# Kernel optimization log

Measured on AMD Instinct MI355X. Metric: run time of the kernel, lower is better.

The kernel has to match this reference:

```python
import jax, jax.numpy as jnp
import numpy as np

N = 50000
E = 800000
D_IN = 64
D_E = 32
H = 128
EPS = 1e-5


def _seg_mean(msgs, dst, n):
    s = jax.ops.segment_sum(msgs, dst, num_segments=n)
    c = jax.ops.segment_sum(jnp.ones((dst.shape[0], 1), msgs.dtype), dst, num_segments=n)
    return s / jnp.maximum(c, 1.0)


def _bn(h, g, b, m, v):
    return g * (h - m) * jax.lax.rsqrt(v + EPS) + b


def setup_inputs() -> dict:
    key = jax.random.key(0)
    ks = jax.random.split(key, 32)
    inp = {
        "x": jax.random.normal(ks[0], (N, D_IN), jnp.float32),
        "edge_index_0": jax.random.randint(ks[1], (2, E), 0, N),
        "edge_index_1": jax.random.randint(ks[2], (2, E), 0, N),
        "edge_index_2": jax.random.randint(ks[3], (2, E), 0, N),
        "edge_attr_0": jax.random.normal(ks[4], (E, D_E), jnp.float32),
        # conv1: Linear(D_IN + D_E -> H)
        "W1": jax.random.normal(ks[5], (H, D_IN + D_E), jnp.float32) * 0.1,
        "b1": jnp.zeros((H,), jnp.float32),
        "g1": jnp.ones((H,), jnp.float32), "be1": jnp.zeros((H,), jnp.float32),
        "m1": jax.random.normal(ks[6], (H,), jnp.float32) * 0.1,
        "v1": jax.random.uniform(ks[7], (H,), jnp.float32) + 0.5,
        # SAGEConv2: lin_l (bias) on aggregated neighbors + lin_r (no bias) on self
        "Wl2": jax.random.normal(ks[8], (H, H), jnp.float32) * 0.1,
        "bl2": jnp.zeros((H,), jnp.float32),
        "Wr2": jax.random.normal(ks[9], (H, H), jnp.float32) * 0.1,
        "g2": jnp.ones((H,), jnp.float32), "be2": jnp.zeros((H,), jnp.float32),
        "m2": jax.random.normal(ks[10], (H,), jnp.float32) * 0.1,
        "v2": jax.random.uniform(ks[11], (H,), jnp.float32) + 0.5,
        # SAGEConv3
        "Wl3": jax.random.normal(ks[12], (H, H), jnp.float32) * 0.1,
        "bl3": jnp.zeros((H,), jnp.float32),
        "Wr3": jax.random.normal(ks[13], (H, H), jnp.float32) * 0.1,
        "g3": jnp.ones((H,), jnp.float32), "be3": jnp.zeros((H,), jnp.float32),
        "m3": jax.random.normal(ks[14], (H,), jnp.float32) * 0.1,
        "v3": jax.random.uniform(ks[15], (H,), jnp.float32) + 0.5,
        # mlp: Linear(H + D_IN -> 64) -> ReLU -> Linear(64 -> 1)
        "W4": jax.random.normal(ks[16], (64, H + D_IN), jnp.float32) * 0.1,
        "b4": jnp.zeros((64,), jnp.float32),
        "W5": jax.random.normal(ks[17], (1, 64), jnp.float32) * 0.1,
        "b5": jnp.zeros((1,), jnp.float32),
    }
    return inp


def reference(x, edge_index_0, edge_index_1, edge_index_2, edge_attr_0,
              W1, b1, g1, be1, m1, v1,
              Wl2, bl2, Wr2, g2, be2, m2, v2,
              Wl3, bl3, Wr3, g3, be3, m3, v3,
              W4, b4, W5, b5):
    n = x.shape[0]
    init = x
    # conv1: gather x_j + edge_attr, concat, linear, mean scatter, relu (update)
    msg = jnp.concatenate([x[edge_index_0[0]], edge_attr_0], axis=-1) @ W1.T + b1  # [E,H]
    h = jax.nn.relu(_seg_mean(msg, edge_index_0[1], n))
    h = jax.nn.relu(_bn(h, g1, be1, m1, v1))  # dropout: eval (identity)
    # conv2: SAGEConv = lin_l(mean_j x_j) + lin_r(x)
    agg = _seg_mean(h[edge_index_1[0]], edge_index_1[1], n)
    h = agg @ Wl2.T + bl2 + h @ Wr2.T
    h = jax.nn.relu(_bn(h, g2, be2, m2, v2))
    # conv3
    agg = _seg_mean(h[edge_index_2[0]], edge_index_2[1], n)
    h = agg @ Wl3.T + bl3 + h @ Wr3.T
    h = jax.nn.relu(_bn(h, g3, be3, m3, v3))
    # readout mlp on [h, initial_embedding]
    z = jnp.concatenate([h, init], axis=1)
    z = jax.nn.relu(z @ W4.T + b4)
    out = (z @ W5.T + b5).squeeze(-1)  # [N]
    return out
```

## Files before the change

### kernel.cpp

```cpp
#include <hip/hip_runtime.h>
#include <hip/hip_bf16.h>
#include <stdint.h>

#define NN 50000
#define NE 800000
#define EPS 1e-5f

#define KB 196
#define SH 8
#define NPB 256
#define RCAP 4500
#define PT2 2048
#define NT2 391
#define GP3 (3 * NT2)
#define GCVT ((3290112 + 255) / 256)

typedef __attribute__((ext_vector_type(8))) short bf16x8;
typedef __attribute__((ext_vector_type(4))) float floatx4;

static __device__ __forceinline__ float bf2f(unsigned int u){
  union { unsigned int i; float f; } c; c.i = u << 16; return c.f;
}
static __device__ __forceinline__ unsigned short f2bf(float f){
  union { float f; unsigned int i; } c; c.f = f;
  unsigned int x = c.i;
  return (unsigned short)((x + 0x7fffu + ((x >> 16) & 1u)) >> 16);
}

#define CVT_X   3200000
#define CVT_W1  3212288
#define CVT_WL2 3228672
#define CVT_WR2 3245056
#define CVT_WL3 3261440
#define CVT_WR3 3277824
#define CVT_END 3290112

__global__ void k_part3cvt(const int* __restrict__ ei0, const int* __restrict__ ei1,
                           const int* __restrict__ ei2, int* __restrict__ gcur,
                           int2* __restrict__ rec,
                           const float* __restrict__ x,  const float* __restrict__ W1,
                           const float* __restrict__ Wl2, const float* __restrict__ Wr2,
                           const float* __restrict__ Wl3, const float* __restrict__ Wr3,
                           const float* __restrict__ W4,
                           unsigned short* __restrict__ xb,  unsigned short* __restrict__ W1b,
                           unsigned short* __restrict__ Wl2b, unsigned short* __restrict__ Wr2b,
                           unsigned short* __restrict__ Wl3b, unsigned short* __restrict__ Wr3b,
                           unsigned short* __restrict__ W4b){
  __shared__ int2 stage[PT2];
  __shared__ int hist[KB], ex[KB], cur[KB], gbase[KB];
  __shared__ int part[256];
  __shared__ int tot;
  int tid = threadIdx.x;

  if(blockIdx.x >= GP3){
    int i = (blockIdx.x - GP3) * 256 + tid;
    if(i >= CVT_END) return;
    if(i < CVT_X)        xb[i] = f2bf(x[i]);
    else if(i < CVT_W1)  W1b[i - CVT_X]    = f2bf(W1[i - CVT_X]);
    else if(i < CVT_WL2) Wl2b[i - CVT_W1]  = f2bf(Wl2[i - CVT_W1]);
    else if(i < CVT_WR2) Wr2b[i - CVT_WL2] = f2bf(Wr2[i - CVT_WL2]);
    else if(i < CVT_WL3) Wl3b[i - CVT_WR2] = f2bf(Wl3[i - CVT_WR2]);
    else if(i < CVT_WR3) Wr3b[i - CVT_WL3] = f2bf(Wr3[i - CVT_WL3]);
    else                 W4b[i - CVT_WR3]  = f2bf(W4[i - CVT_WR3]);
    return;
  }

  int layer = blockIdx.x % 3;
  int tile = (blockIdx.x / 3) * PT2;
  const int* ei = (layer == 0) ? ei0 : ((layer == 1) ? ei1 : ei2);
  int2* recL = rec + (size_t)layer * KB * RCAP;
  int* gcurL = gcur + layer * KB;
  for(int i = tid; i < KB; i += 256) hist[i] = 0;
  __syncthreads();
  int dst[8], pay[8];
  #pragma unroll
  for(int j = 0; j < 8; j++){
    int e = tile + j * 256 + tid;
    if(e < NE){
      dst[j] = ei[NE + e];
      pay[j] = (layer == 0) ? e : ei[e];
      atomicAdd(&hist[dst[j] >> SH], 1);
    }
    else dst[j] = -1;
  }
  __syncthreads();
  int c0 = (tid < KB) ? hist[tid] : 0;
  part[tid] = c0;
  __syncthreads();
  for(int d = 1; d < 256; d <<= 1){
    int v = (tid >= d) ? part[tid - d] : 0;
    __syncthreads();
    part[tid] += v;
    __syncthreads();
  }
  if(tid < KB){
    int e = part[tid] - c0;
    ex[tid] = e; cur[tid] = e;
    gbase[tid] = atomicAdd(&gcurL[tid], c0);
  }
  if(tid == 255) tot = part[255];
  __syncthreads();
  #pragma unroll
  for(int j = 0; j < 8; j++){
    if(dst[j] >= 0){
      int b = dst[j] >> SH;
      int s = atomicAdd(&cur[b], 1);
      stage[s] = make_int2(dst[j], pay[j]);
    }
  }
  __syncthreads();
  for(int s = tid; s < tot; s += 256){
    int2 r = stage[s];
    int b = r.x >> SH;
    recL[b * RCAP + gbase[b] + (s - ex[b])] = r;
  }
}

__global__ void k_build3(const int2* __restrict__ rec, const int* __restrict__ gcnt,
                         const int* __restrict__ ei0,
                         int2* __restrict__ adj2, int* __restrict__ adjI1, int* __restrict__ adjI2,
                         int* __restrict__ rowbeg3, int* __restrict__ deg3){
  __shared__ int cnt[NPB], cur2[NPB];
  __shared__ int part[256];
  int layer = blockIdx.x % 3;
  int b = blockIdx.x / 3;
  int tid = threadIdx.x;
  int n0 = b << SH;
  int nr = gcnt[layer * KB + b];
  const int2* r = rec + ((size_t)layer * KB + b) * RCAP;
  cnt[tid] = 0;
  __syncthreads();
  for(int k = tid; k < nr; k += 256) atomicAdd(&cnt[r[k].x - n0], 1);
  __syncthreads();
  int c0 = cnt[tid];
  part[tid] = c0;
  __syncthreads();
  for(int d = 1; d < 256; d <<= 1){
    int v = (tid >= d) ? part[tid - d] : 0;
    __syncthreads();
    part[tid] += v;
    __syncthreads();
  }
  int base = part[tid] - c0;
  cur2[tid] = base;
  __syncthreads();
  int n = n0 + tid;
  if(n < NN){ rowbeg3[layer * NN + n] = b * RCAP + base; deg3[layer * NN + n] = c0; }
  for(int k = tid; k < nr; k += 256){
    int2 q = r[k];
    int p = atomicAdd(&cur2[q.x - n0], 1);
    if(layer == 0)      adj2[b * RCAP + p]  = make_int2(ei0[q.y], q.y);
    else if(layer == 1) adjI1[b * RCAP + p] = q.y;
    else                adjI2[b * RCAP + p] = q.y;
  }
}

__global__ void k_aggXE(const int* __restrict__ rowbeg, const int* __restrict__ deg,
                        const int2* __restrict__ adj2,
                        const unsigned short* __restrict__ xb, const float* __restrict__ ea,
                        unsigned short* __restrict__ agg){
  int w = (blockIdx.x * blockDim.x + threadIdx.x) >> 6;
  int lane = threadIdx.x & 63;
  if(w >= NN) return;
  int sub = lane >> 4, li = lane & 15;
  int r0 = rowbeg[w], dg = deg[w], r1 = r0 + dg;
  float acc[8] = {0.f,0.f,0.f,0.f,0.f,0.f,0.f,0.f};
  for(int k = r0; k < r1; k += 8){
    int e0 = k + sub, e1 = k + 4 + sub;
    int i0 = e0 < r1 ? e0 : r1 - 1;
    int i1 = e1 < r1 ? e1 : r1 - 1;
    float m0 = e0 < r1 ? 1.f : 0.f;
    float m1 = e1 < r1 ? 1.f : 0.f;
    int2 a0 = adj2[i0], a1 = adj2[i1];
    if(li < 8){
      uint4 v0 = *(const uint4*)(xb + (size_t)a0.x * 64 + li * 8);
      uint4 v1 = *(const uint4*)(xb + (size_t)a1.x * 64 + li * 8);
      acc[0] += m0 * bf2f(v0.x & 0xffffu); acc[1] += m0 * bf2f(v0.x >> 16);
      acc[2] += m0 * bf2f(v0.y & 0xffffu); acc[3] += m0 * bf2f(v0.y >> 16);
      acc[4] += m0 * bf2f(v0.z & 0xffffu); acc[5] += m0 * bf2f(v0.z >> 16);
      acc[6] += m0 * bf2f(v0.w & 0xffffu); acc[7] += m0 * bf2f(v0.w >> 16);
      acc[0] += m1 * bf2f(v1.x & 0xffffu); acc[1] += m1 * bf2f(v1.x >> 16);
      acc[2] += m1 * bf2f(v1.y & 0xffffu); acc[3] += m1 * bf2f(v1.y >> 16);
      acc[4] += m1 * bf2f(v1.z & 0xffffu); acc[5] += m1 * bf2f(v1.z >> 16);
      acc[6] += m1 * bf2f(v1.w & 0xffffu); acc[7] += m1 * bf2f(v1.w >> 16);
    } else {
      int j = li - 8;
      float4 p0 = *(const float4*)(ea + (size_t)a0.y * 32 + j * 4);
      float4 p1 = *(const float4*)(ea + (size_t)a1.y * 32 + j * 4);
      acc[0] += m0 * p0.x; acc[1] += m0 * p0.y;
      acc[2] += m0 * p0.z; acc[3] += m0 * p0.w;
      acc[0] += m1 * p1.x; acc[1] += m1 * p1.y;
      acc[2] += m1 * p1.z; acc[3] += m1 * p1.w;
    }
  }
  #pragma unroll
  for(int d = 16; d < 64; d <<= 1){
    #pragma unroll
    for(int i = 0; i < 8; i++) acc[i] += __shfl_xor(acc[i], d, 64);
  }
  if(sub == 0){
    float inv = 1.0f / (float)(dg > 0 ? dg : 1);
    if(li < 8){
      unsigned int q0 = (unsigned int)f2bf(acc[0]*inv) | ((unsigned int)f2bf(acc[1]*inv) << 16);
      unsigned int q1 = (unsigned int)f2bf(acc[2]*inv) | ((unsigned int)f2bf(acc[3]*inv) << 16);
      unsigned int q2 = (unsigned int)f2bf(acc[4]*inv) | ((unsigned int)f2bf(acc[5]*inv) << 16);
      unsigned int q3 = (unsigned int)f2bf(acc[6]*inv) | ((unsigned int)f2bf(acc[7]*inv) << 16);
      *(uint4*)(agg + (size_t)w * 96 + li * 8) = make_uint4(q0, q1, q2, q3);
    } else {
      int j = li - 8;
      unsigned int q0 = (unsigned int)f2bf(acc[0]*inv) | ((unsigned int)f2bf(acc[1]*inv) << 16);
      unsigned int q1 = (unsigned int)f2bf(acc[2]*inv) | ((unsigned int)f2bf(acc[3]*inv) << 16);
      *(uint2*)(agg + (size_t)w * 96 + 64 + j * 4) = make_uint2(q0, q1);
    }
  }
}

__global__ void k_aggH(const int* __restrict__ rowbeg, const int* __restrict__ deg,
                       const int* __restrict__ adj,
                       const unsigned short* __restrict__ h, unsigned short* __restrict__ agg){
  int w = (blockIdx.x * blockDim.x + threadIdx.x) >> 6;
  int lane = threadIdx.x & 63;
  if(w >= NN) return;
  int sub = lane >> 4, li = lane & 15;
  int r0 = rowbeg[w], dg = deg[w], r1 = r0 + dg;
  float acc[8] = {0.f,0.f,0.f,0.f,0.f,0.f,0.f,0.f};
  for(int k = r0; k < r1; k += 8){
    int e0 = k + sub, e1 = k + 4 + sub;
    int i0 = e0 < r1 ? e0 : r1 - 1;
    int i1 = e1 < r1 ? e1 : r1 - 1;
    float m0 = e0 < r1 ? 1.f : 0.f;
    float m1 = e1 < r1 ? 1.f : 0.f;
    int s0 = adj[i0], s1 = adj[i1];
    uint4 v0 = *(const uint4*)(h + (size_t)s0 * 128 + li * 8);
    uint4 v1 = *(const uint4*)(h + (size_t)s1 * 128 + li * 8);
    acc[0] += m0 * bf2f(v0.x & 0xffffu); acc[1] += m0 * bf2f(v0.x >> 16);
    acc[2] += m0 * bf2f(v0.y & 0xffffu); acc[3] += m0 * bf2f(v0.y >> 16);
    acc[4] += m0 * bf2f(v0.z & 0xffffu); acc[5] += m0 * bf2f(v0.z >> 16);
    acc[6] += m0 * bf2f(v0.w & 0xffffu); acc[7] += m0 * bf2f(v0.w >> 16);
    acc[0] += m1 * bf2f(v1.x & 0xffffu); acc[1] += m1 * bf2f(v1.x >> 16);
    acc[2] += m1 * bf2f(v1.y & 0xffffu); acc[3] += m1 * bf2f(v1.y >> 16);
    acc[4] += m1 * bf2f(v1.z & 0xffffu); acc[5] += m1 * bf2f(v1.z >> 16);
    acc[6] += m1 * bf2f(v1.w & 0xffffu); acc[7] += m1 * bf2f(v1.w >> 16);
  }
  #pragma unroll
  for(int d = 16; d < 64; d <<= 1){
    #pragma unroll
    for(int i = 0; i < 8; i++) acc[i] += __shfl_xor(acc[i], d, 64);
  }
  if(sub == 0){
    float inv = 1.0f / (float)(dg > 0 ? dg : 1);
    unsigned int p0 = (unsigned int)f2bf(acc[0]*inv) | ((unsigned int)f2bf(acc[1]*inv) << 16);
    unsigned int p1 = (unsigned int)f2bf(acc[2]*inv) | ((unsigned int)f2bf(acc[3]*inv) << 16);
    unsigned int p2 = (unsigned int)f2bf(acc[4]*inv) | ((unsigned int)f2bf(acc[5]*inv) << 16);
    unsigned int p3 = (unsigned int)f2bf(acc[6]*inv) | ((unsigned int)f2bf(acc[7]*inv) << 16);
    *(uint4*)(agg + (size_t)w * 128 + li * 8) = make_uint4(p0, p1, p2, p3);
  }
}

__global__ void k_lin1(const unsigned short* __restrict__ agg, const unsigned short* __restrict__ W1,
                       const float* __restrict__ b1,
                       const float* __restrict__ g1, const float* __restrict__ be1,
                       const float* __restrict__ m1, const float* __restrict__ v1,
                       const int* __restrict__ deg, unsigned short* __restrict__ h1){
  int wave = (blockIdx.x * blockDim.x + threadIdx.x) >> 6;
  int lane = threadIdx.x & 63;
  int mt = wave >> 3, nt = wave & 7;
  if(mt >= 3125) return;
  int node0 = mt * 16;
  int col = lane & 15, quad = lane >> 4;
  int o = nt * 16 + col;
  int arow = node0 + col;
  floatx4 acc = {0.f, 0.f, 0.f, 0.f};
  #pragma unroll
  for(int kc = 0; kc < 3; kc++){
    bf16x8 a = *(const bf16x8*)(agg + arow * 96 + kc * 32 + quad * 8);
    bf16x8 b = *(const bf16x8*)(W1 + o * 96 + kc * 32 + quad * 8);
    acc = __builtin_amdgcn_mfma_f32_16x16x32_bf16(a, b, acc, 0, 0, 0);
  }
  float bb = b1[o];
  float sc = g1[o] * rsqrtf(v1[o] + EPS);
  float mv = m1[o], bev = be1[o];
  #pragma unroll
  for(int r = 0; r < 4; r++){
    int node = node0 + quad * 4 + r;
    float pre = (deg[node] > 0) ? (acc[r] + bb) : 0.0f;
    float t = fmaxf(pre, 0.f);
    float bn = sc * (t - mv) + bev;
    h1[node * 128 + o] = f2bf(fmaxf(bn, 0.f));
  }
}

__global__ void k_sage(const unsigned short* __restrict__ agg, const unsigned short* __restrict__ hin,
                       const unsigned short* __restrict__ Wl, const float* __restrict__ bl,
                       const unsigned short* __restrict__ Wr,
                       const float* __restrict__ g, const float* __restrict__ be,
                       const float* __restrict__ m, const float* __restrict__ v,
                       unsigned short* __restrict__ hout){
  int wave = (blockIdx.x * blockDim.x + threadIdx.x) >> 6;
  int lane = threadIdx.x & 63;
  int mt = wave >> 3, nt = wave & 7;
  if(mt >= 3125) return;
  int node0 = mt * 16;
  int col = lane & 15, quad = lane >> 4;
  int o = nt * 16 + col;
  int arow = node0 + col;
  floatx4 acc = {0.f, 0.f, 0.f, 0.f};
  #pragma unroll
  for(int kc = 0; kc < 4; kc++){
    bf16x8 a = *(const bf16x8*)(agg + arow * 128 + kc * 32 + quad * 8);
    bf16x8 b = *(const bf16x8*)(Wl + o * 128 + kc * 32 + quad * 8);
    acc = __builtin_amdgcn_mfma_f32_16x16x32_bf16(a, b, acc, 0, 0, 0);
  }
  #pragma unroll
  for(int kc = 0; kc < 4; kc++){
    bf16x8 a = *(const bf16x8*)(hin + arow * 128 + kc * 32 + quad * 8);
    bf16x8 b = *(const bf16x8*)(Wr + o * 128 + kc * 32 + quad * 8);
    acc = __builtin_amdgcn_mfma_f32_16x16x32_bf16(a, b, acc, 0, 0, 0);
  }
  float blv = bl[o];
  float sc = g[o] * rsqrtf(v[o] + EPS);
  float mv = m[o], bev = be[o];
  #pragma unroll
  for(int r = 0; r < 4; r++){
    int node = node0 + quad * 4 + r;
    float pre = acc[r] + blv;
    float bn = sc * (pre - mv) + bev;
    hout[node * 128 + o] = f2bf(fmaxf(bn, 0.f));
  }
}

__global__ void k_readout(const unsigned short* __restrict__ h3, const unsigned short* __restrict__ xb,
                          const unsigned short* __restrict__ W4, const float* __restrict__ b4,
                          const float* __restrict__ W5, const float* __restrict__ b5,
                          float* __restrict__ out){
  int wave = (blockIdx.x * blockDim.x + threadIdx.x) >> 6;
  int lane = threadIdx.x & 63;
  if(wave >= 3125) return;
  int node0 = wave * 16;
  int col = lane & 15, quad = lane >> 4;
  int arow = node0 + col;
  float partial[4] = {0.f, 0.f, 0.f, 0.f};
  #pragma unroll
  for(int nt = 0; nt < 4; nt++){
    int o = nt * 16 + col;
    floatx4 acc = {0.f, 0.f, 0.f, 0.f};
    #pragma unroll
    for(int kc = 0; kc < 4; kc++){
      bf16x8 a = *(const bf16x8*)(h3 + arow * 128 + kc * 32 + quad * 8);
      bf16x8 b = *(const bf16x8*)(W4 + o * 192 + kc * 32 + quad * 8);
      acc = __builtin_amdgcn_mfma_f32_16x16x32_bf16(a, b, acc, 0, 0, 0);
    }
    #pragma unroll
    for(int kc = 0; kc < 2; kc++){
      bf16x8 a = *(const bf16x8*)(xb + arow * 64 + kc * 32 + quad * 8);
      bf16x8 b = *(const bf16x8*)(W4 + o * 192 + 128 + kc * 32 + quad * 8);
      acc = __builtin_amdgcn_mfma_f32_16x16x32_bf16(a, b, acc, 0, 0, 0);
    }
    float bb = b4[o];
    float w5 = W5[o];
    #pragma unroll
    for(int r = 0; r < 4; r++)
      partial[r] += fmaxf(acc[r] + bb, 0.f) * w5;
  }
  #pragma unroll
  for(int d = 1; d < 16; d <<= 1){
    #pragma unroll
    for(int r = 0; r < 4; r++)
      partial[r] += __shfl_xor(partial[r], d, 64);
  }
  if(col == 0){
    float b5f = b5[0];
    #pragma unroll
    for(int r = 0; r < 4; r++)
      out[node0 + quad * 4 + r] = partial[r] + b5f;
  }
}

extern "C" void kernel_launch(void* const* d_in, const int* in_sizes, int n_in,
                              void* d_out, int out_size, void* d_ws, size_t ws_size,
                              hipStream_t stream) {
  const float* x   = (const float*)d_in[0];
  const int* ei0   = (const int*)d_in[1];
  const int* ei1   = (const int*)d_in[2];
  const int* ei2   = (const int*)d_in[3];
  const float* ea  = (const float*)d_in[4];
  const float* W1  = (const float*)d_in[5];
  const float* b1  = (const float*)d_in[6];
  const float* g1  = (const float*)d_in[7];
  const float* be1 = (const float*)d_in[8];
  const float* m1  = (const float*)d_in[9];
  const float* v1  = (const float*)d_in[10];
  const float* Wl2 = (const float*)d_in[11];
  const float* bl2 = (const float*)d_in[12];
  const float* Wr2 = (const float*)d_in[13];
  const float* g2  = (const float*)d_in[14];
  const float* be2 = (const float*)d_in[15];
  const float* m2  = (const float*)d_in[16];
  const float* v2  = (const float*)d_in[17];
  const float* Wl3 = (const float*)d_in[18];
  const float* bl3 = (const float*)d_in[19];
  const float* Wr3 = (const float*)d_in[20];
  const float* g3  = (const float*)d_in[21];
  const float* be3 = (const float*)d_in[22];
  const float* m3  = (const float*)d_in[23];
  const float* v3  = (const float*)d_in[24];
  const float* W4  = (const float*)d_in[25];
  const float* b4  = (const float*)d_in[26];
  const float* W5  = (const float*)d_in[27];
  const float* b5  = (const float*)d_in[28];

  char* ws = (char*)d_ws;
  size_t off = 0;
  auto alloc = [&](size_t bytes) -> void* {
    void* p = (void*)(ws + off);
    off += (bytes + 255) & ~(size_t)255;
    return p;
  };
  int* gcur    = (int*)alloc(3 * KB * sizeof(int));
  int* rowbeg3 = (int*)alloc(3 * NN * sizeof(int));
  int* deg3    = (int*)alloc(3 * NN * sizeof(int));
  char* uni    = (char*)alloc((size_t)3 * NN * 128 * 2);
  int2* adj2   = (int2*)alloc((size_t)KB * RCAP * 8);
  int* adjI1   = (int*)alloc((size_t)KB * RCAP * 4);
  int* adjI2   = (int*)alloc((size_t)KB * RCAP * 4);
  unsigned short* agg1 = (unsigned short*)alloc((size_t)NN * 96 * 2);
  unsigned short* xb   = (unsigned short*)alloc((size_t)NN * 64 * 2);
  unsigned short* W1b  = (unsigned short*)alloc(12288 * 2);
  unsigned short* Wl2b = (unsigned short*)alloc(16384 * 2);
  unsigned short* Wr2b = (unsigned short*)alloc(16384 * 2);
  unsigned short* Wl3b = (unsigned short*)alloc(16384 * 2);
  unsigned short* Wr3b = (unsigned short*)alloc(16384 * 2);
  unsigned short* W4b  = (unsigned short*)alloc(12288 * 2);

  int2* recDS = (int2*)uni;
  unsigned short* h1   = (unsigned short*)uni;
  unsigned short* aggH = h1 + (size_t)NN * 128;
  unsigned short* h2   = h1 + (size_t)2 * NN * 128;
  unsigned short* h3   = h1;

  int* rb0 = rowbeg3;            int* dg0 = deg3;
  int* rb1 = rowbeg3 + NN;       int* dg1 = deg3 + NN;
  int* rb2 = rowbeg3 + 2 * NN;   int* dg2 = deg3 + 2 * NN;

  const int gB3   = 3 * KB;
  const int gAgg  = (NN * 64) / 256;
  const int gTile = (3125 * 8 * 64) / 256;
  const int gRead = (3125 * 64 + 255) / 256;

  hipMemsetAsync(gcur, 0, 3 * KB * sizeof(int), stream);

  k_part3cvt<<<GP3 + GCVT, 256, 0, stream>>>(ei0, ei1, ei2, gcur, recDS,
                                             x, W1, Wl2, Wr2, Wl3, Wr3, W4,
                                             xb, W1b, Wl2b, Wr2b, Wl3b, Wr3b, W4b);
  k_build3<<<gB3, 256, 0, stream>>>(recDS, gcur, ei0, adj2, adjI1, adjI2, rowbeg3, deg3);

  k_aggXE<<<gAgg, 256, 0, stream>>>(rb0, dg0, adj2, xb, ea, agg1);
  k_lin1<<<gTile, 256, 0, stream>>>(agg1, W1b, b1, g1, be1, m1, v1, dg0, h1);

  k_aggH<<<gAgg, 256, 0, stream>>>(rb1, dg1, adjI1, h1, aggH);
  k_sage<<<gTile, 256, 0, stream>>>(aggH, h1, Wl2b, bl2, Wr2b, g2, be2, m2, v2, h2);

  k_aggH<<<gAgg, 256, 0, stream>>>(rb2, dg2, adjI2, h2, aggH);
  k_sage<<<gTile, 256, 0, stream>>>(aggH, h2, Wl3b, bl3, Wr3b, g3, be3, m3, v3, h3);

  k_readout<<<gRead, 256, 0, stream>>>(h3, xb, W4b, b4, W5, b5, (float*)d_out);

  (void)in_sizes; (void)n_in; (void)out_size; (void)ws_size;
}
```

Baseline: 498.4 us.

## Fuse neighbor aggregation with per-layer GEMM via shared-memory tiles

Each aggregation kernel now processes 16 nodes per 1024-thread block, writes the mean-aggregated rows into a shared-memory tile, and then eight of the waves run the MFMA linear layer plus BN/ReLU directly from that tile. This removes the global round trip of the aggregated features and three kernel launches. The bf16 conversion is split out of the partition kernel into its own launch, and that launch also zeroes the counters, replacing the memset. Half the waves sit idle during the GEMM phase, and the large blocks may reduce occupancy flexibility.

Result: faster. 470.9 us (-5.5%).

```diff
diff --git a/kernel.cpp b/kernel.cpp
--- a/kernel.cpp
+++ b/kernel.cpp
@@ -12,8 +12,9 @@
 #define RCAP 4500
 #define PT2 2048
 #define NT2 391
-#define GP3 (3 * NT2)
-#define GCVT ((3290112 + 255) / 256)
+
+#define PADL 104
+#define PADS 136
 
 typedef __attribute__((ext_vector_type(8))) short bf16x8;
 typedef __attribute__((ext_vector_type(4))) float floatx4;
@@ -34,37 +35,34 @@
 #define CVT_WL3 3261440
 #define CVT_WR3 3277824
 #define CVT_END 3290112
-
-__global__ void k_part3cvt(const int* __restrict__ ei0, const int* __restrict__ ei1,
-                           const int* __restrict__ ei2, int* __restrict__ gcur,
-                           int2* __restrict__ rec,
-                           const float* __restrict__ x,  const float* __restrict__ W1,
-                           const float* __restrict__ Wl2, const float* __restrict__ Wr2,
-                           const float* __restrict__ Wl3, const float* __restrict__ Wr3,
-                           const float* __restrict__ W4,
-                           unsigned short* __restrict__ xb,  unsigned short* __restrict__ W1b,
-                           unsigned short* __restrict__ Wl2b, unsigned short* __restrict__ Wr2b,
-                           unsigned short* __restrict__ Wl3b, unsigned short* __restrict__ Wr3b,
-                           unsigned short* __restrict__ W4b){
+__global__ void k_cvt_all(const float* __restrict__ x,  const float* __restrict__ W1,
+                          const float* __restrict__ Wl2, const float* __restrict__ Wr2,
+                          const float* __restrict__ Wl3, const float* __restrict__ Wr3,
+                          const float* __restrict__ W4,
+                          unsigned short* __restrict__ xb,  unsigned short* __restrict__ W1b,
+                          unsigned short* __restrict__ Wl2b, unsigned short* __restrict__ Wr2b,
+                          unsigned short* __restrict__ Wl3b, unsigned short* __restrict__ Wr3b,
+                          unsigned short* __restrict__ W4b, int* __restrict__ gcur){
+  int i = blockIdx.x * 256 + threadIdx.x;
+  if(i >= CVT_END) return;
+  if(i < 3 * KB) gcur[i] = 0;
+  if(i < CVT_X)        xb[i] = f2bf(x[i]);
+  else if(i < CVT_W1)  W1b[i - CVT_X]    = f2bf(W1[i - CVT_X]);
+  else if(i < CVT_WL2) Wl2b[i - CVT_W1]  = f2bf(Wl2[i - CVT_W1]);
+  else if(i < CVT_WR2) Wr2b[i - CVT_WL2] = f2bf(Wr2[i - CVT_WL2]);
+  else if(i < CVT_WL3) Wl3b[i - CVT_WR2] = f2bf(Wl3[i - CVT_WR2]);
+  else if(i < CVT_WR3) Wr3b[i - CVT_WL3] = f2bf(Wr3[i - CVT_WL3]);
+  else                 W4b[i - CVT_WR3]  = f2bf(W4[i - CVT_WR3]);
+}
+
+__global__ void k_part3(const int* __restrict__ ei0, const int* __restrict__ ei1,
+                        const int* __restrict__ ei2, int* __restrict__ gcur,
+                        int2* __restrict__ rec){
   __shared__ int2 stage[PT2];
   __shared__ int hist[KB], ex[KB], cur[KB], gbase[KB];
   __shared__ int part[256];
   __shared__ int tot;
   int tid = threadIdx.x;
-
-  if(blockIdx.x >= GP3){
-    int i = (blockIdx.x - GP3) * 256 + tid;
-    if(i >= CVT_END) return;
-    if(i < CVT_X)        xb[i] = f2bf(x[i]);
-    else if(i < CVT_W1)  W1b[i - CVT_X]    = f2bf(W1[i - CVT_X]);
-    else if(i < CVT_WL2) Wl2b[i - CVT_W1]  = f2bf(Wl2[i - CVT_W1]);
-    else if(i < CVT_WR2) Wr2b[i - CVT_WL2] = f2bf(Wr2[i - CVT_WL2]);
-    else if(i < CVT_WL3) Wl3b[i - CVT_WR2] = f2bf(Wl3[i - CVT_WR2]);
-    else if(i < CVT_WR3) Wr3b[i - CVT_WL3] = f2bf(Wr3[i - CVT_WL3]);
-    else                 W4b[i - CVT_WR3]  = f2bf(W4[i - CVT_WR3]);
-    return;
-  }
-
   int layer = blockIdx.x % 3;
   int tile = (blockIdx.x / 3) * PT2;
   const int* ei = (layer == 0) ? ei0 : ((layer == 1) ? ei1 : ei2);
@@ -155,13 +153,19 @@
   }
 }
 
-__global__ void k_aggXE(const int* __restrict__ rowbeg, const int* __restrict__ deg,
+__global__ __launch_bounds__(1024) void k_aggXElin(
+                        const int* __restrict__ rowbeg, const int* __restrict__ deg,
                         const int2* __restrict__ adj2,
                         const unsigned short* __restrict__ xb, const float* __restrict__ ea,
-                        unsigned short* __restrict__ agg){
-  int w = (blockIdx.x * blockDim.x + threadIdx.x) >> 6;
-  int lane = threadIdx.x & 63;
-  if(w >= NN) return;
+                        const unsigned short* __restrict__ W1, const float* __restrict__ b1,
+                        const float* __restrict__ g1, const float* __restrict__ be1,
+                        const float* __restrict__ m1, const float* __restrict__ v1,
+                        unsigned short* __restrict__ h1){
+  __shared__ unsigned short sA[16][PADL];
+  int tid = threadIdx.x;
+  int wv = tid >> 6, lane = tid & 63;
+  int node0 = blockIdx.x * 16;
+  int w = node0 + wv;
   int sub = lane >> 4, li = lane & 15;
   int r0 = rowbeg[w], dg = deg[w], r1 = r0 + dg;
   float acc[8] = {0.f,0.f,0.f,0.f,0.f,0.f,0.f,0.f};
@@ -170,7 +174,7 @@
     int i0 = e0 < r1 ? e0 : r1 - 1;
     int i1 = e1 < r1 ? e1 : r1 - 1;
     float m0 = e0 < r1 ? 1.f : 0.f;
-    float m1 = e1 < r1 ? 1.f : 0.f;
+    float m1f = e1 < r1 ? 1.f : 0.f;
     int2 a0 = adj2[i0], a1 = adj2[i1];
     if(li < 8){
       uint4 v0 = *(const uint4*)(xb + (size_t)a0.x * 64 + li * 8);
@@ -179,18 +183,18 @@
       acc[2] += m0 * bf2f(v0.y & 0xffffu); acc[3] += m0 * bf2f(v0.y >> 16);
       acc[4] += m0 * bf2f(v0.z & 0xffffu); acc[5] += m0 * bf2f(v0.z >> 16);
       acc[6] += m0 * bf2f(v0.w & 0xffffu); acc[7] += m0 * bf2f(v0.w >> 16);
-      acc[0] += m1 * bf2f(v1.x & 0xffffu); acc[1] += m1 * bf2f(v1.x >> 16);
-      acc[2] += m1 * bf2f(v1.y & 0xffffu); acc[3] += m1 * bf2f(v1.y >> 16);
-      acc[4] += m1 * bf2f(v1.z & 0xffffu); acc[5] += m1 * bf2f(v1.z >> 16);
-      acc[6] += m1 * bf2f(v1.w & 0xffffu); acc[7] += m1 * bf2f(v1.w >> 16);
+      acc[0] += m1f * bf2f(v1.x & 0xffffu); acc[1] += m1f * bf2f(v1.x >> 16);
+      acc[2] += m1f * bf2f(v1.y & 0xffffu); acc[3] += m1f * bf2f(v1.y >> 16);
+      acc[4] += m1f * bf2f(v1.z & 0xffffu); acc[5] += m1f * bf2f(v1.z >> 16);
+      acc[6] += m1f * bf2f(v1.w & 0xffffu); acc[7] += m1f * bf2f(v1.w >> 16);
     } else {
       int j = li - 8;
       float4 p0 = *(const float4*)(ea + (size_t)a0.y * 32 + j * 4);
       float4 p1 = *(const float4*)(ea + (size_t)a1.y * 32 + j * 4);
       acc[0] += m0 * p0.x; acc[1] += m0 * p0.y;
       acc[2] += m0 * p0.z; acc[3] += m0 * p0.w;
-      acc[0] += m1 * p1.x; acc[1] += m1 * p1.y;
-      acc[2] += m1 * p1.z; acc[3] += m1 * p1.w;
+      acc[0] += m1f * p1.x; acc[1] += m1f * p1.y;
+      acc[2] += m1f * p1.z; acc[3] += m1f * p1.w;
     }
   }
   #pragma unroll
@@ -205,22 +209,53 @@
       unsigned int q1 = (unsigned int)f2bf(acc[2]*inv) | ((unsigned int)f2bf(acc[3]*inv) << 16);
       unsigned int q2 = (unsigned int)f2bf(acc[4]*inv) | ((unsigned int)f2bf(acc[5]*inv) << 16);
       unsigned int q3 = (unsigned int)f2bf(acc[6]*inv) | ((unsigned int)f2bf(acc[7]*inv) << 16);
-      *(uint4*)(agg + (size_t)w * 96 + li * 8) = make_uint4(q0, q1, q2, q3);
+      *(uint4*)&sA[wv][li * 8] = make_uint4(q0, q1, q2, q3);
     } else {
       int j = li - 8;
       unsigned int q0 = (unsigned int)f2bf(acc[0]*inv) | ((unsigned int)f2bf(acc[1]*inv) << 16);
       unsigned int q1 = (unsigned int)f2bf(acc[2]*inv) | ((unsigned int)f2bf(acc[3]*inv) << 16);
-      *(uint2*)(agg + (size_t)w * 96 + 64 + j * 4) = make_uint2(q0, q1);
-    }
-  }
-}
-
-__global__ void k_aggH(const int* __restrict__ rowbeg, const int* __restrict__ deg,
+      *(uint2*)&sA[wv][64 + j * 4] = make_uint2(q0, q1);
+    }
+  }
+  __syncthreads();
+  if(wv < 8){
+    int col = lane & 15, quad = lane >> 4;
+    int o = wv * 16 + col;
+    floatx4 acc2 = {0.f, 0.f, 0.f, 0.f};
+    #pragma unroll
+    for(int kc = 0; kc < 3; kc++){
+      bf16x8 a = *(const bf16x8*)&sA[col][kc * 32 + quad * 8];
+      bf16x8 b = *(const bf16x8*)(W1 + o * 96 + kc * 32 + quad * 8);
+      acc2 = __builtin_amdgcn_mfma_f32_16x16x32_bf16(a, b, acc2, 0, 0, 0);
+    }
+    float bb = b1[o];
+    float sc = g1[o] * rsqrtf(v1[o] + EPS);
+    float mv = m1[o], bev = be1[o];
+    #pragma unroll
+    for(int r = 0; r < 4; r++){
+      int node = node0 + quad * 4 + r;
+      float pre = (deg[node] > 0) ? (acc2[r] + bb) : 0.0f;
+      float t = fmaxf(pre, 0.f);
+      float bn = sc * (t - mv) + bev;
+      h1[node * 128 + o] = f2bf(fmaxf(bn, 0.f));
+    }
+  }
+}
+
+__global__ __launch_bounds__(1024) void k_aggsage(
+                       const int* __restrict__ rowbeg, const int* __restrict__ deg,
                        const int* __restrict__ adj,
-                       const unsigned short* __restrict__ h, unsigned short* __restrict__ agg){
-  int w = (blockIdx.x * blockDim.x + threadIdx.x) >> 6;
-  int lane = threadIdx.x & 63;
-  if(w >= NN) return;
+                       const unsigned short* __restrict__ hin,
+                       const unsigned short* __restrict__ Wl, const float* __restrict__ bl,
+                       const unsigned short* __restrict__ Wr,
+                       const float* __restrict__ g, const float* __restrict__ be,
+                       const float* __restrict__ m, const float* __restrict__ v,
+                       unsigned short* __restrict__ hout){
+  __shared__ unsigned short sA[16][PADS];
+  int tid = threadIdx.x;
+  int wv = tid >> 6, lane = tid & 63;
+  int node0 = blockIdx.x * 16;
+  int w = node0 + wv;
   int sub = lane >> 4, li = lane & 15;
   int r0 = rowbeg[w], dg = deg[w], r1 = r0 + dg;
   float acc[8] = {0.f,0.f,0.f,0.f,0.f,0.f,0.f,0.f};
@@ -229,18 +264,18 @@
     int i0 = e0 < r1 ? e0 : r1 - 1;
     int i1 = e1 < r1 ? e1 : r1 - 1;
     float m0 = e0 < r1 ? 1.f : 0.f;
-    float m1 = e1 < r1 ? 1.f : 0.f;
+    float m1f = e1 < r1 ? 1.f : 0.f;
     int s0 = adj[i0], s1 = adj[i1];
-    uint4 v0 = *(const uint4*)(h + (size_t)s0 * 128 + li * 8);
-    uint4 v1 = *(const uint4*)(h + (size_t)s1 * 128 + li * 8);
+    uint4 v0 = *(const uint4*)(hin + (size_t)s0 * 128 + li * 8);
+    uint4 v1 = *(const uint4*)(hin + (size_t)s1 * 128 + li * 8);
     acc[0] += m0 * bf2f(v0.x & 0xffffu); acc[1] += m0 * bf2f(v0.x >> 16);
     acc[2] += m0 * bf2f(v0.y & 0xffffu); acc[3] += m0 * bf2f(v0.y >> 16);
     acc[4] += m0 * bf2f(v0.z & 0xffffu); acc[5] += m0 * bf2f(v0.z >> 16);
     acc[6] += m0 * bf2f(v0.w & 0xffffu); acc[7] += m0 * bf2f(v0.w >> 16);
-    acc[0] += m1 * bf2f(v1.x & 0xffffu); acc[1] += m1 * bf2f(v1.x >> 16);
-    acc[2] += m1 * bf2f(v1.y & 0xffffu); acc[3] += m1 * bf2f(v1.y >> 16);
-    acc[4] += m1 * bf2f(v1.z & 0xffffu); acc[5] += m1 * bf2f(v1.z >> 16);
-    acc[6] += m1 * bf2f(v1.w & 0xffffu); acc[7] += m1 * bf2f(v1.w >> 16);
+    acc[0] += m1f * bf2f(v1.x & 0xffffu); acc[1] += m1f * bf2f(v1.x >> 16);
+    acc[2] += m1f * bf2f(v1.y & 0xffffu); acc[3] += m1f * bf2f(v1.y >> 16);
+    acc[4] += m1f * bf2f(v1.z & 0xffffu); acc[5] += m1f * bf2f(v1.z >> 16);
+    acc[6] += m1f * bf2f(v1.w & 0xffffu); acc[7] += m1f * bf2f(v1.w >> 16);
   }
   #pragma unroll
   for(int d = 16; d < 64; d <<= 1){
@@ -253,79 +288,36 @@
     unsigned int p1 = (unsigned int)f2bf(acc[2]*inv) | ((unsigned int)f2bf(acc[3]*inv) << 16);
     unsigned int p2 = (unsigned int)f2bf(acc[4]*inv) | ((unsigned int)f2bf(acc[5]*inv) << 16);
     unsigned int p3 = (unsigned int)f2bf(acc[6]*inv) | ((unsigned int)f2bf(acc[7]*inv) << 16);
-    *(uint4*)(agg + (size_t)w * 128 + li * 8) = make_uint4(p0, p1, p2, p3);
-  }
-}
-
-__global__ void k_lin1(const unsigned short* __restrict__ agg, const unsigned short* __restrict__ W1,
-                       const float* __restrict__ b1,
-                       const float* __restrict__ g1, const float* __restrict__ be1,
-                       const float* __restrict__ m1, const float* __restrict__ v1,
-                       const int* __restrict__ deg, unsigned short* __restrict__ h1){
-  int wave = (blockIdx.x * blockDim.x + threadIdx.x) >> 6;
-  int lane = threadIdx.x & 63;
-  int mt = wave >> 3, nt = wave & 7;
-  if(mt >= 3125) return;
-  int node0 = mt * 16;
-  int col = lane & 15, quad = lane >> 4;
-  int o = nt * 16 + col;
-  int arow = node0 + col;
-  floatx4 acc = {0.f, 0.f, 0.f, 0.f};
-  #pragma unroll
-  for(int kc = 0; kc < 3; kc++){
-    bf16x8 a = *(const bf16x8*)(agg + arow * 96 + kc * 32 + quad * 8);
-    bf16x8 b = *(const bf16x8*)(W1 + o * 96 + kc * 32 + quad * 8);
-    acc = __builtin_amdgcn_mfma_f32_16x16x32_bf16(a, b, acc, 0, 0, 0);
-  }
-  float bb = b1[o];
-  float sc = g1[o] * rsqrtf(v1[o] + EPS);
-  float mv = m1[o], bev = be1[o];
-  #pragma unroll
-  for(int r = 0; r < 4; r++){
-    int node = node0 + quad * 4 + r;
-    float pre = (deg[node] > 0) ? (acc[r] + bb) : 0.0f;
-    float t = fmaxf(pre, 0.f);
-    float bn = sc * (t - mv) + bev;
-    h1[node * 128 + o] = f2bf(fmaxf(bn, 0.f));
-  }
-}
-
-__global__ void k_sage(const unsigned short* __restrict__ agg, const unsigned short* __restrict__ hin,
-                       const unsigned short* __restrict__ Wl, const float* __restrict__ bl,
-                       const unsigned short* __restrict__ Wr,
-                       const float* __restrict__ g, const float* __restrict__ be,
-                       const float* __restrict__ m, const float* __restrict__ v,
-                       unsigned short* __restrict__ hout){
-  int wave = (blockIdx.x * blockDim.x + threadIdx.x) >> 6;
-  int lane = threadIdx.x & 63;
-  int mt = wave >> 3, nt = wave & 7;
-  if(mt >= 3125) return;
-  int node0 = mt * 16;
-  int col = lane & 15, quad = lane >> 4;
-  int o = nt * 16 + col;
-  int arow = node0 + col;
-  floatx4 acc = {0.f, 0.f, 0.f, 0.f};
-  #pragma unroll
-  for(int kc = 0; kc < 4; kc++){
-    bf16x8 a = *(const bf16x8*)(agg + arow * 128 + kc * 32 + quad * 8);
-    bf16x8 b = *(const bf16x8*)(Wl + o * 128 + kc * 32 + quad * 8);
-    acc = __builtin_amdgcn_mfma_f32_16x16x32_bf16(a, b, acc, 0, 0, 0);
-  }
-  #pragma unroll
-  for(int kc = 0; kc < 4; kc++){
-    bf16x8 a = *(const bf16x8*)(hin + arow * 128 + kc * 32 + quad * 8);
-    bf16x8 b = *(const bf16x8*)(Wr + o * 128 + kc * 32 + quad * 8);
-    acc = __builtin_amdgcn_mfma_f32_16x16x32_bf16(a, b, acc, 0, 0, 0);
-  }
-  float blv = bl[o];
-  float sc = g[o] * rsqrtf(v[o] + EPS);
-  float mv = m[o], bev = be[o];
-  #pragma unroll
-  for(int r = 0; r < 4; r++){
-    int node = node0 + quad * 4 + r;
-    float pre = acc[r] + blv;
-    float bn = sc * (pre - mv) + bev;
-    hout[node * 128 + o] = f2bf(fmaxf(bn, 0.f));
+    *(uint4*)&sA[wv][li * 8] = make_uint4(p0, p1, p2, p3);
+  }
+  __syncthreads();
+  if(wv < 8){
+    int col = lane & 15, quad = lane >> 4;
+    int o = wv * 16 + col;
+    int arow = node0 + col;
+    floatx4 acc2 = {0.f, 0.f, 0.f, 0.f};
+    #pragma unroll
+    for(int kc = 0; kc < 4; kc++){
+      bf16x8 a = *(const bf16x8*)&sA[col][kc * 32 + quad * 8];
+      bf16x8 b = *(const bf16x8*)(Wl + o * 128 + kc * 32 + quad * 8);
+      acc2 = __builtin_amdgcn_mfma_f32_16x16x32_bf16(a, b, acc2, 0, 0, 0);
+    }
+    #pragma unroll
+    for(int kc = 0; kc < 4; kc++){
+      bf16x8 a = *(const bf16x8*)(hin + arow * 128 + kc * 32 + quad * 8);
+      bf16x8 b = *(const bf16x8*)(Wr + o * 128 + kc * 32 + quad * 8);
+      acc2 = __builtin_amdgcn_mfma_f32_16x16x32_bf16(a, b, acc2, 0, 0, 0);
+    }
+    float blv = bl[o];
+    float sc = g[o] * rsqrtf(v[o] + EPS);
+    float mv = m[o], bev = be[o];
+    #pragma unroll
+    for(int r = 0; r < 4; r++){
+      int node = node0 + quad * 4 + r;
+      float pre = acc2[r] + blv;
+      float bn = sc * (pre - mv) + bev;
+      hout[node * 128 + o] = f2bf(fmaxf(bn, 0.f));
+    }
   }
 }
 
@@ -419,11 +411,10 @@
   int* gcur    = (int*)alloc(3 * KB * sizeof(int));
   int* rowbeg3 = (int*)alloc(3 * NN * sizeof(int));
   int* deg3    = (int*)alloc(3 * NN * sizeof(int));
-  char* uni    = (char*)alloc((size_t)3 * NN * 128 * 2);
+  char* uni    = (char*)alloc((size_t)2 * NN * 128 * 2);
   int2* adj2   = (int2*)alloc((size_t)KB * RCAP * 8);
   int* adjI1   = (int*)alloc((size_t)KB * RCAP * 4);
   int* adjI2   = (int*)alloc((size_t)KB * RCAP * 4);
-  unsigned short* agg1 = (unsigned short*)alloc((size_t)NN * 96 * 2);
   unsigned short* xb   = (unsigned short*)alloc((size_t)NN * 64 * 2);
   unsigned short* W1b  = (unsigned short*)alloc(12288 * 2);
   unsigned short* Wl2b = (unsigned short*)alloc(16384 * 2);
@@ -434,34 +425,33 @@
 
   int2* recDS = (int2*)uni;
   unsigned short* h1   = (unsigned short*)uni;
-  unsigned short* aggH = h1 + (size_t)NN * 128;
-  unsigned short* h2   = h1 + (size_t)2 * NN * 128;
+  unsigned short* h2   = h1 + (size_t)NN * 128;
   unsigned short* h3   = h1;
 
   int* rb0 = rowbeg3;            int* dg0 = deg3;
   int* rb1 = rowbeg3 + NN;       int* dg1 = deg3 + NN;
   int* rb2 = rowbeg3 + 2 * NN;   int* dg2 = deg3 + 2 * NN;
 
+  const int gP3   = 3 * NT2;
   const int gB3   = 3 * KB;
-  const int gAgg  = (NN * 64) / 256;
-  const int gTile = (3125 * 8 * 64) / 256;
+  const int gFuse = NN / 16;
   const int gRead = (3125 * 64 + 255) / 256;
-
-  hipMemsetAsync(gcur, 0, 3 * KB * sizeof(int), stream);
-
-  k_part3cvt<<<GP3 + GCVT, 256, 0, stream>>>(ei0, ei1, ei2, gcur, recDS,
-                                             x, W1, Wl2, Wr2, Wl3, Wr3, W4,
-                                             xb, W1b, Wl2b, Wr2b, Wl3b, Wr3b, W4b);
+  const int gCvt  = (CVT_END + 255) / 256;
+
+  k_cvt_all<<<gCvt, 256, 0, stream>>>(x, W1, Wl2, Wr2, Wl3, Wr3, W4,
+                                      xb, W1b, Wl2b, Wr2b, Wl3b, Wr3b, W4b, gcur);
+
+  k_part3<<<gP3, 256, 0, stream>>>(ei0, ei1, ei2, gcur, recDS);
   k_build3<<<gB3, 256, 0, stream>>>(recDS, gcur, ei0, adj2, adjI1, adjI2, rowbeg3, deg3);
 
-  k_aggXE<<<gAgg, 256, 0, stream>>>(rb0, dg0, adj2, xb, ea, agg1);
-  k_lin1<<<gTile, 256, 0, stream>>>(agg1, W1b, b1, g1, be1, m1, v1, dg0, h1);
-
-  k_aggH<<<gAgg, 256, 0, stream>>>(rb1, dg1, adjI1, h1, aggH);
-  k_sage<<<gTile, 256, 0, stream>>>(aggH, h1, Wl2b, bl2, Wr2b, g2, be2, m2, v2, h2);
-
-  k_aggH<<<gAgg, 256, 0, stream>>>(rb2, dg2, adjI2, h2, aggH);
-  k_sage<<<gTile, 256, 0, stream>>>(aggH, h2, Wl3b, bl3, Wr3b, g3, be3, m3, v3, h3);
+  k_aggXElin<<<gFuse, 1024, 0, stream>>>(rb0, dg0, adj2, xb, ea,
+                                         W1b, b1, g1, be1, m1, v1, h1);
+
+  k_aggsage<<<gFuse, 1024, 0, stream>>>(rb1, dg1, adjI1, h1,
+                                        Wl2b, bl2, Wr2b, g2, be2, m2, v2, h2);
+
+  k_aggsage<<<gFuse, 1024, 0, stream>>>(rb2, dg2, adjI2, h2,
+                                        Wl3b, bl3, Wr3b, g3, be3, m3, v3, h3);
 
   k_readout<<<gRead, 256, 0, stream>>>(h3, xb, W4b, b4, W5, b5, (float*)d_out);
 
```
